# Kernel optimization log

Measured on AMD Instinct MI355X. Metric: run time of the kernel, lower is better.

Reference implementation:

```python
import jax, jax.numpy as jnp
import numpy as np

IN_FEATURES = 4096
OUT_FEATURES = 4096

def setup_inputs() -> dict:
    key = jax.random.key(0)
    kx, kw, kb = jax.random.split(key, 3)
    x = jax.random.normal(kx, (8192, IN_FEATURES), dtype=jnp.float32)
    weight = jax.random.normal(kw, (OUT_FEATURES, IN_FEATURES), dtype=jnp.float32)
    bias = jax.random.normal(kb, (OUT_FEATURES,), dtype=jnp.float32)
    return {"x": x, "weight": weight, "bias": bias}

def reference(x, weight, bias):
    # Binarize weights to {-1, 0, +1} via sign, then dense linear: y = x @ sign(W)^T + b
    w_bin = jnp.sign(weight)
    return jnp.einsum('bi,oi->bo', x, w_bin) + bias
```

## Files before the change

### kernel.cpp

```cpp
#include <hip/hip_runtime.h>
#include <hip/hip_bf16.h>
#include <stdint.h>

#define M_DIM 8192
#define N_DIM 4096
#define K_DIM 4096

#define NT 64

using i32x4 = __attribute__((ext_vector_type(4))) int;

typedef const __attribute__((address_space(1))) void glb_void_t;
typedef __attribute__((address_space(3))) void lds_void_t;

__device__ __forceinline__ void async16(const void* g, void* l) {
    __builtin_amdgcn_global_load_lds((glb_void_t*)(uintptr_t)g,
                                     (lds_void_t*)(uint32_t)(uintptr_t)l,
                                     16, 0, 0);
}

__device__ __forceinline__ int sgn_i8(float f) {
    union { float f; uint32_t u; } v; v.f = f;
    if ((v.u & 0x7FFFFFFFu) == 0u) return 0;
    return (v.u >> 31) ? -1 : 1;
}


__global__ void convert_w_kernel(const float* __restrict__ w,
                                 unsigned char* __restrict__ wq, int n4) {
    int stride = gridDim.x * blockDim.x;
    for (int i = blockIdx.x * blockDim.x + threadIdx.x; i < n4; i += stride) {
        float4 v = ((const float4*)w)[i];
        uint32_t o = ((uint32_t)(uint8_t)sgn_i8(v.x)) |
                     ((uint32_t)(uint8_t)sgn_i8(v.y) << 8) |
                     ((uint32_t)(uint8_t)sgn_i8(v.z) << 16) |
                     ((uint32_t)(uint8_t)sgn_i8(v.w) << 24);
        ((uint32_t*)wq)[i] = o;
    }
}


__global__ __launch_bounds__(256)
void convert_x_kernel(const float* __restrict__ x,
                      unsigned char* __restrict__ xq,
                      float* __restrict__ scales) {
    const int row = blockIdx.x;
    const int tid = threadIdx.x;
    const float4* xr = (const float4*)(x + (size_t)row * K_DIM);
    float4 v[4];
    float m = 0.f;
    #pragma unroll
    for (int j = 0; j < 4; ++j) {
        v[j] = xr[j * 256 + tid];
        m = fmaxf(m, fmaxf(fmaxf(fabsf(v[j].x), fabsf(v[j].y)),
                           fmaxf(fabsf(v[j].z), fabsf(v[j].w))));
    }
    #pragma unroll
    for (int off = 32; off >= 1; off >>= 1)
        m = fmaxf(m, __shfl_xor(m, off));
    __shared__ float wmax[4];
    if ((tid & 63) == 0) wmax[tid >> 6] = m;
    __syncthreads();
    m = fmaxf(fmaxf(wmax[0], wmax[1]), fmaxf(wmax[2], wmax[3]));
    const float inv = (m > 0.f) ? 127.0f / m : 0.f;
    if (tid == 0) scales[row] = (m > 0.f) ? m / 127.0f : 0.f;
    uint32_t* oq = (uint32_t*)(xq + (size_t)row * K_DIM);
    #pragma unroll
    for (int j = 0; j < 4; ++j) {
        float q0 = fminf(fmaxf(rintf(v[j].x * inv), -127.f), 127.f);
        float q1 = fminf(fmaxf(rintf(v[j].y * inv), -127.f), 127.f);
        float q2 = fminf(fmaxf(rintf(v[j].z * inv), -127.f), 127.f);
        float q3 = fminf(fmaxf(rintf(v[j].w * inv), -127.f), 127.f);
        uint32_t o = ((uint32_t)(uint8_t)(int)q0) |
                     ((uint32_t)(uint8_t)(int)q1 << 8) |
                     ((uint32_t)(uint8_t)(int)q2 << 16) |
                     ((uint32_t)(uint8_t)(int)q3 << 24);
        oq[j * 256 + tid] = o;
    }
}


#define BAR   __builtin_amdgcn_s_barrier()
#define VM4   asm volatile("s_waitcnt vmcnt(4)" ::: "memory")
#define VM0   asm volatile("s_waitcnt vmcnt(0)" ::: "memory")

#define RDA(BUFV, MLO) \
    _Pragma("unroll") for (int mm = 0; mm < 4; ++mm) \
        a[mm] = rdfrag((BUFV), wm, ((MLO) + mm) * 16);

#define RDB(BUFV) \
    _Pragma("unroll") for (int nn = 0; nn < 4; ++nn) \
        b[nn] = rdfrag((BUFV), sectB, rB + nn * 16);

#define MM16(MB) \
    __builtin_amdgcn_s_setprio(1); \
    _Pragma("unroll") for (int mm = 0; mm < 4; ++mm) \
    _Pragma("unroll") for (int nn = 0; nn < 4; ++nn) \
        acc[(MB) + mm][nn] = __builtin_amdgcn_mfma_i32_16x16x64_i8( \
            a[mm], b[nn], acc[(MB) + mm][nn], 0, 0, 0); \
    __builtin_amdgcn_s_setprio(0);

#define KT(T, S, VMW) do { \
    const int cb_ = (T) % 3; const int pb_ = ((T) + 2) % 3; \
    if (S) { \
        stage(pb_, 0, xq, brow,       ((T) + 2) * 64); \
        stage(pb_, 1, xq, brow + 128, ((T) + 2) * 64); \
        stage(pb_, 2, wq, bcol,       ((T) + 2) * 64); \
        stage(pb_, 3, wq, bcol + 128, ((T) + 2) * 64); \
    } \
    RDB(cb_) RDA(cb_, 0) \
    MM16(0) \
    RDA(cb_, 4) \
    MM16(4) \
    VMW; \
    BAR; \
} while (0)

__global__ __launch_bounds__(512, 2)
void gemm_bin_kernel(const unsigned char* __restrict__ xq,
                     const unsigned char* __restrict__ wq,
                     const float* __restrict__ scales,
                     const float* __restrict__ bias,
                     float* __restrict__ out) {
    __shared__ __align__(16) unsigned char lds[3][4][8192];

    const int tid  = threadIdx.x;
    const int wid  = tid >> 6;
    const int lane = tid & 63;

    const int bid  = blockIdx.x;
    const int swzb = (bid & 7) * 64 + (bid >> 3);
    const int brow = (swzb >> 4) * 256;
    const int bcol = (swzb & 15) * 256;

    const int wm = wid >> 2;
    const int wn = wid & 3;
    const int fr  = lane & 15;
    const int g16 = (lane >> 4) << 4;
    const int sw  = ((lane >> 1) & 3) << 4;
    const int sectB = 2 + (wn >> 1);
    const int rB    = (wn & 1) * 64;

    i32x4 acc[8][4] = {};
    i32x4 a[4], b[4];

    const int srow = tid >> 2;
    const int scol = ((tid & 3) ^ ((tid >> 3) & 3)) * 16;
    auto stage = [&](int bufv, int sect, const unsigned char* g, int row0, int k0) {
        async16(g + (size_t)(row0 + srow) * K_DIM + (k0 + scol),
                &lds[bufv][sect][0] + tid * 16);
    };

    auto rdfrag = [&](int bufv, int sect, int rbase) -> i32x4 {
        const unsigned char* base = &lds[bufv][sect][0];
        return *(const i32x4*)(base + (rbase + fr) * 64 + (g16 ^ sw));
    };

    stage(0, 0, xq, brow,        0);
    stage(0, 1, xq, brow + 128,  0);
    stage(0, 2, wq, bcol,        0);
    stage(0, 3, wq, bcol + 128,  0);
    stage(1, 0, xq, brow,       64);
    stage(1, 1, xq, brow + 128, 64);
    stage(1, 2, wq, bcol,       64);
    stage(1, 3, wq, bcol + 128, 64);
    VM4;
    BAR;

    for (int t = 0; t < NT - 2; ++t) KT(t, 1, VM4);
    KT(NT - 2, 0, VM0);
    KT(NT - 1, 0, (void)0);

    const int wrow = wm * 128, wcol = wn * 64;
    float bv[4];
    #pragma unroll
    for (int n = 0; n < 4; ++n) bv[n] = bias[bcol + wcol + n * 16 + fr];
    const int r4 = (lane >> 4) * 4;
    #pragma unroll
    for (int m = 0; m < 8; ++m) {
        #pragma unroll
        for (int rr = 0; rr < 4; ++rr) {
            const int row = brow + wrow + m * 16 + r4 + rr;
            const float sc = scales[row];
            float* orow = out + (size_t)row * N_DIM + bcol + wcol;
            #pragma unroll
            for (int n = 0; n < 4; ++n)
                orow[n * 16 + fr] = (float)acc[m][n][rr] * sc + bv[n];
        }
    }
}


__global__ void naive_kernel(const float* __restrict__ x,
                             const float* __restrict__ w,
                             const float* __restrict__ bias,
                             float* __restrict__ out) {
    const size_t total = (size_t)M_DIM * N_DIM;
    for (size_t idx = (size_t)blockIdx.x * blockDim.x + threadIdx.x; idx < total;
         idx += (size_t)gridDim.x * blockDim.x) {
        const size_t row = idx >> 12;
        const size_t col = idx & 4095;
        const float4* xr  = (const float4*)(x + row * K_DIM);
        const float4* wrp = (const float4*)(w + col * K_DIM);
        float s = 0.f;
        for (int k = 0; k < K_DIM / 4; ++k) {
            float4 a = xr[k], bq = wrp[k];
            s += a.x * (bq.x > 0.f ? 1.f : (bq.x < 0.f ? -1.f : 0.f));
            s += a.y * (bq.y > 0.f ? 1.f : (bq.y < 0.f ? -1.f : 0.f));
            s += a.z * (bq.z > 0.f ? 1.f : (bq.z < 0.f ? -1.f : 0.f));
            s += a.w * (bq.w > 0.f ? 1.f : (bq.w < 0.f ? -1.f : 0.f));
        }
        out[idx] = s + bias[col];
    }
}

extern "C" void kernel_launch(void* const* d_in, const int* in_sizes, int n_in,
                              void* d_out, int out_size, void* d_ws, size_t ws_size,
                              hipStream_t stream) {
    const float* x    = (const float*)d_in[0];
    const float* w    = (const float*)d_in[1];
    const float* bias = (const float*)d_in[2];
    float* out = (float*)d_out;

    const size_t xq_bytes = (size_t)M_DIM * K_DIM;
    const size_t wq_bytes = (size_t)N_DIM * K_DIM;
    const size_t sc_bytes = (size_t)M_DIM * sizeof(float);

    if (ws_size >= xq_bytes + wq_bytes + sc_bytes) {
        unsigned char* xq = (unsigned char*)d_ws;
        unsigned char* wq = (unsigned char*)d_ws + xq_bytes;
        float* scales     = (float*)((char*)d_ws + xq_bytes + wq_bytes);
        convert_w_kernel<<<2048, 256, 0, stream>>>(w, wq,
            (int)((size_t)N_DIM * K_DIM / 4));
        convert_x_kernel<<<M_DIM, 256, 0, stream>>>(x, xq, scales);
        gemm_bin_kernel<<<dim3((M_DIM / 256) * (N_DIM / 256)), dim3(512), 0, stream>>>(
            xq, wq, scales, bias, out);
    } else {
        naive_kernel<<<4096, 256, 0, stream>>>(x, w, bias, out);
    }
}
```

Before: 187.1 us.

## Deepen LDS ring to four stages and double-buffer MFMA fragments in registers

The shared-memory ring grows from three to four K-tile stages, so each global-to-LDS load is issued three tiles ahead. All A and B fragments for the next tile are read from LDS into a second register set while the MFMAs for the current tile run, ping-ponging between two fragment sets. The goal is to hide LDS read latency and global load latency behind matrix-core work. In exchange, LDS use rises to 128KB per block and the extra fragment registers raise register pressure.

After: 185.1 us. About the same (-1.0%).

```diff
diff --git a/kernel.cpp b/kernel.cpp
--- a/kernel.cpp
+++ b/kernel.cpp
@@ -84,36 +84,29 @@
 #define VM4   asm volatile("s_waitcnt vmcnt(4)" ::: "memory")
 #define VM0   asm volatile("s_waitcnt vmcnt(0)" ::: "memory")
 
-#define RDA(BUFV, MLO) \
-    _Pragma("unroll") for (int mm = 0; mm < 4; ++mm) \
-        a[mm] = rdfrag((BUFV), wm, ((MLO) + mm) * 16);
-
-#define RDB(BUFV) \
+#define STG(T) do { \
+    const int pb_ = (T) & 3; \
+    stage(pb_, 0, xq, brow,       (T) * 64); \
+    stage(pb_, 1, xq, brow + 128, (T) * 64); \
+    stage(pb_, 2, wq, bcol,       (T) * 64); \
+    stage(pb_, 3, wq, bcol + 128, (T) * 64); \
+} while (0)
+
+#define RDSET(AV, BV, T) do { \
+    const int rb_ = (T) & 3; \
     _Pragma("unroll") for (int nn = 0; nn < 4; ++nn) \
-        b[nn] = rdfrag((BUFV), sectB, rB + nn * 16);
-
-#define MM16(MB) \
+        BV[nn] = rdfrag(rb_, sectB, rB + nn * 16); \
+    _Pragma("unroll") for (int mm = 0; mm < 8; ++mm) \
+        AV[mm] = rdfrag(rb_, wm, mm * 16); \
+} while (0)
+
+#define MMA(AV, BV) do { \
     __builtin_amdgcn_s_setprio(1); \
-    _Pragma("unroll") for (int mm = 0; mm < 4; ++mm) \
+    _Pragma("unroll") for (int mm = 0; mm < 8; ++mm) \
     _Pragma("unroll") for (int nn = 0; nn < 4; ++nn) \
-        acc[(MB) + mm][nn] = __builtin_amdgcn_mfma_i32_16x16x64_i8( \
-            a[mm], b[nn], acc[(MB) + mm][nn], 0, 0, 0); \
-    __builtin_amdgcn_s_setprio(0);
-
-#define KT(T, S, VMW) do { \
-    const int cb_ = (T) % 3; const int pb_ = ((T) + 2) % 3; \
-    if (S) { \
-        stage(pb_, 0, xq, brow,       ((T) + 2) * 64); \
-        stage(pb_, 1, xq, brow + 128, ((T) + 2) * 64); \
-        stage(pb_, 2, wq, bcol,       ((T) + 2) * 64); \
-        stage(pb_, 3, wq, bcol + 128, ((T) + 2) * 64); \
-    } \
-    RDB(cb_) RDA(cb_, 0) \
-    MM16(0) \
-    RDA(cb_, 4) \
-    MM16(4) \
-    VMW; \
-    BAR; \
+        acc[mm][nn] = __builtin_amdgcn_mfma_i32_16x16x64_i8( \
+            AV[mm], BV[nn], acc[mm][nn], 0, 0, 0); \
+    __builtin_amdgcn_s_setprio(0); \
 } while (0)
 
 __global__ __launch_bounds__(512, 2)
@@ -122,7 +115,7 @@
                      const float* __restrict__ scales,
                      const float* __restrict__ bias,
                      float* __restrict__ out) {
-    __shared__ __align__(16) unsigned char lds[3][4][8192];
+    __shared__ __align__(16) unsigned char lds[4][4][8192];
 
     const int tid  = threadIdx.x;
     const int wid  = tid >> 6;
@@ -142,7 +135,7 @@
     const int rB    = (wn & 1) * 64;
 
     i32x4 acc[8][4] = {};
-    i32x4 a[4], b[4];
+    i32x4 a0[8], b0[4], a1[8], b1[4];
 
     const int srow = tid >> 2;
     const int scol = ((tid & 3) ^ ((tid >> 3) & 3)) * 16;
@@ -156,20 +149,20 @@
         return *(const i32x4*)(base + (rbase + fr) * 64 + (g16 ^ sw));
     };
 
-    stage(0, 0, xq, brow,        0);
-    stage(0, 1, xq, brow + 128,  0);
-    stage(0, 2, wq, bcol,        0);
-    stage(0, 3, wq, bcol + 128,  0);
-    stage(1, 0, xq, brow,       64);
-    stage(1, 1, xq, brow + 128, 64);
-    stage(1, 2, wq, bcol,       64);
-    stage(1, 3, wq, bcol + 128, 64);
+    STG(0); STG(1); STG(2);
     VM4;
     BAR;
-
-    for (int t = 0; t < NT - 2; ++t) KT(t, 1, VM4);
-    KT(NT - 2, 0, VM0);
-    KT(NT - 1, 0, (void)0);
+    RDSET(a0, b0, 0);
+
+    for (int tt = 0; tt < 30; ++tt) {
+        const int T = tt * 2;
+        STG(T + 3); RDSET(a1, b1, T + 1); MMA(a0, b0); VM4; BAR;
+        STG(T + 4); RDSET(a0, b0, T + 2); MMA(a1, b1); VM4; BAR;
+    }
+    STG(63); RDSET(a1, b1, 61); MMA(a0, b0); VM4; BAR;
+    RDSET(a0, b0, 62); MMA(a1, b1); VM0; BAR;
+    RDSET(a1, b1, 63); MMA(a0, b0);
+    MMA(a1, b1);
 
     const int wrow = wm * 128, wcol = wn * 64;
     float bv[4];
```
